# Optimization experiments

Hardware: AMD Instinct MI355X
Metric: run time of the kernel (lower is better)

Reference implementation:

```python
import jax, jax.numpy as jnp
import numpy as np

P = 10  # pred_num_conn (capped by max_pred_num_conn), component 0 = background
L = 6   # label_num_conn, component 0 = background
N, H, W = 4, 1024, 1024


def setup_inputs() -> dict:
    key = jax.random.key(0)
    k1, k2, k3 = jax.random.split(key, 3)
    pred = jax.random.uniform(k1, (N, H, W), dtype=jnp.float32)
    pred_conn = jax.random.randint(k2, (N, H, W), 0, P, dtype=jnp.int32)
    label_conn = jax.random.randint(k3, (N, H, W), 0, L, dtype=jnp.int32)
    return {"pred": pred, "pred_conn": pred_conn, "label_conn": label_conn}


def _image_sc_loss(pred_i, pconn, lconn):
    # pred_i: [H,W] float, pconn/lconn: [H,W] int component ids
    ph = jax.nn.one_hot(pconn, P, dtype=pred_i.dtype)   # [H,W,P]
    lh = jax.nn.one_hot(lconn, L, dtype=pred_i.dtype)   # [H,W,L]
    pm = ph * pred_i[..., None]                          # pred_j = mask_j * pred
    inter = jnp.einsum('hwl,hwp->lp', lh, pm)            # [L,P] intersection areas
    pred_area = jnp.sum(pm, axis=(0, 1))                 # [P]
    label_area = jnp.sum(lh, axis=(0, 1))                # [L]
    union = label_area[:, None] + pred_area[None, :] - inter
    safe_union = jnp.where(union == 0, 1.0, union)
    # compute_iou: 0 if intersect==0, 1 if union==0, else inter/union
    iou = jnp.where(inter == 0, 0.0,
                    jnp.where(union == 0, 1.0, inter / safe_union))
    ious = iou[1:, 1:]                                   # drop background comps -> [L-1, P-1]
    pair_conn = jnp.sum(ious, axis=1)                    # sum of nonzero ious per label comp
    pair_num = jnp.sum(ious != 0, axis=1).astype(pred_i.dtype)
    contrib = jnp.where(pair_num > 0,
                        pair_conn / jnp.where(pair_num > 0, pair_num, 1.0), 0.0)
    pair_conn_sum = jnp.sum(contrib)
    pred_col_sum = jnp.sum(ious, axis=0)                 # [P-1]
    lone_pred_num = jnp.sum(pred_col_sum == 0).astype(pred_i.dtype)
    real_label_num = jnp.asarray(L - 1, pred_i.dtype)
    img_connectivity = pair_conn_sum / (real_label_num + lone_pred_num)
    return 1.0 - img_connectivity                        # sc_loss for one class (class_num=1)


def reference(pred, pred_conn, label_conn):
    sc = jax.vmap(_image_sc_loss)(pred, pred_conn, label_conn)  # [N]
    return jnp.mean(sc)
```

## Files before the change

kernel.cpp:

```cpp
#include <hip/hip_runtime.h>

#define PP 10
#define LL 6
#define NIMG 4
#define HW (1024*1024)
#define BINS 66
#define NB 60
#define BX 512
#define TPB 128
#define ITERS 4


__global__ __launch_bounds__(TPB, 2) void accum_kernel(
    const float* __restrict__ pred,
    const int*   __restrict__ pconn,
    const int*   __restrict__ lconn,
    float*       __restrict__ ws)
{
    __shared__ float sb[NB * TPB];
    __shared__ float scnt[2][8];

    const int tid = threadIdx.x;
    const int img = blockIdx.y;
    const size_t base = (size_t)img * HW;

    {
        float4* sb4 = (float4*)sb;
        for (int i = tid; i < NB * TPB / 4; i += TPB)
            sb4[i] = make_float4(0.f, 0.f, 0.f, 0.f);
    }
    __syncthreads();

    const float4* __restrict__ p4  = (const float4*)(pred  + base);
    const int4*   __restrict__ pc4 = (const int4*)(pconn + base);
    const int4*   __restrict__ lc4 = (const int4*)(lconn + base);

    const int v0 = blockIdx.x * TPB + tid;
    const int stride = BX * TPB;

    float4 p[ITERS]; int4 pc[ITERS], lc[ITERS];
#pragma unroll
    for (int i = 0; i < ITERS; ++i) {
        const int v = v0 + i * stride;
        p[i]  = p4[v];
        pc[i] = pc4[v];
        lc[i] = lc4[v];
    }

    float cnt[LL];
#pragma unroll
    for (int l = 0; l < LL; ++l) cnt[l] = 0.0f;

#pragma unroll
    for (int i = 0; i < ITERS; ++i) {
#pragma unroll
        for (int l = 0; l < LL; ++l)
            cnt[l] += (float)((lc[i].x == l) + (lc[i].y == l)
                            + (lc[i].z == l) + (lc[i].w == l));
        sb[(lc[i].x * PP + pc[i].x) * TPB + tid] += p[i].x;
        sb[(lc[i].y * PP + pc[i].y) * TPB + tid] += p[i].y;
        sb[(lc[i].z * PP + pc[i].z) * TPB + tid] += p[i].z;
        sb[(lc[i].w * PP + pc[i].w) * TPB + tid] += p[i].w;
    }
    __syncthreads();

    float* wout = ws + ((size_t)img * BX + blockIdx.x) * BINS;

#pragma unroll
    for (int l = 0; l < LL; ++l) {
        float s = cnt[l];
        s += __shfl_down(s, 32, 64); s += __shfl_down(s, 16, 64);
        s += __shfl_down(s,  8, 64); s += __shfl_down(s,  4, 64);
        s += __shfl_down(s,  2, 64); s += __shfl_down(s,  1, 64);
        if ((tid & 63) == 0) scnt[tid >> 6][l] = s;
    }

    {
        const int b = tid >> 1, h = tid & 1;
        if (b < NB) {
            const float* col = sb + b * TPB + 64 * h;
            float s = 0.0f;
#pragma unroll
            for (int i = 0; i < 16; ++i) {
                const int ii = ((i + tid) & 15) * 4;
                const float4 t4 = *(const float4*)(col + ii);
                s += t4.x + t4.y + t4.z + t4.w;
            }
            s += __shfl_down(s, 1, 64);
            if (h == 0) wout[b] = s;
        }
    }
    __syncthreads();
    if (tid < LL) wout[NB + tid] = scnt[0][tid] + scnt[1][tid];
}

__global__ __launch_bounds__(1024) void finalize_kernel(
    const float* __restrict__ ws, float* __restrict__ out)
{
    __shared__ float part[4][NIMG * BINS];
    __shared__ float red[NIMG * BINS];
    __shared__ float contrib[NIMG];
    const int t = threadIdx.x;

    for (int T = t; T < 4 * NIMG * BINS; T += 1024) {
        const int ib = T >> 2, sub = T & 3;
        const int img = ib / BINS, b = ib % BINS;
        const float* basep = ws + ((size_t)img * BX + sub) * BINS + b;
        float s = 0.0f;
#pragma unroll 8
        for (int j = 0; j < BX / 4; ++j) s += basep[(size_t)j * 4 * BINS];
        part[sub][ib] = s;
    }
    __syncthreads();

    if (t < NIMG * BINS)
        red[t] = part[0][t] + part[1][t] + part[2][t] + part[3][t];
    __syncthreads();

    if (t < NIMG) {
        const float* b = red + t * BINS;
        float inter[LL][PP], pred_area[PP], label_area[LL];
        for (int p = 0; p < PP; ++p) pred_area[p] = 0.0f;
        for (int l = 0; l < LL; ++l) {
            label_area[l] = b[NB + l];
            for (int p = 0; p < PP; ++p) {
                inter[l][p] = b[l * PP + p];
                pred_area[p] += inter[l][p];
            }
        }
        float ious[LL][PP];
        for (int l = 1; l < LL; ++l) {
            for (int p = 1; p < PP; ++p) {
                float in = inter[l][p];
                float un = label_area[l] + pred_area[p] - in;
                float iou;
                if (in == 0.0f)      iou = 0.0f;
                else if (un == 0.0f) iou = 1.0f;
                else                 iou = in / un;
                ious[l][p] = iou;
            }
        }
        float pair_conn_sum = 0.0f;
        for (int l = 1; l < LL; ++l) {
            float pc = 0.0f; int pn = 0;
            for (int p = 1; p < PP; ++p) {
                pc += ious[l][p];
                pn += (ious[l][p] != 0.0f) ? 1 : 0;
            }
            if (pn > 0) pair_conn_sum += pc / (float)pn;
        }
        int lone = 0;
        for (int p = 1; p < PP; ++p) {
            float cs = 0.0f;
            for (int l = 1; l < LL; ++l) cs += ious[l][p];
            lone += (cs == 0.0f) ? 1 : 0;
        }
        contrib[t] = 1.0f - pair_conn_sum / (5.0f + (float)lone);
    }
    __syncthreads();
    if (t == 0)
        out[0] = (contrib[0] + contrib[1] + contrib[2] + contrib[3]) * 0.25f;
}

extern "C" void kernel_launch(void* const* d_in, const int* in_sizes, int n_in,
                              void* d_out, int out_size, void* d_ws, size_t ws_size,
                              hipStream_t stream) {
    const float* pred  = (const float*)d_in[0];
    const int*   pconn = (const int*)d_in[1];
    const int*   lconn = (const int*)d_in[2];
    float* out = (float*)d_out;
    float* ws  = (float*)d_ws;

    dim3 grid(BX, NIMG);
    accum_kernel<<<grid, TPB, 0, stream>>>(pred, pconn, lconn, ws);

    finalize_kernel<<<1, 1024, 0, stream>>>(ws, out);
}
```

Measured before the change: 109.6 us.

## Replace shared-memory scatter histogram with per-thread register one-hot FMA accumulation

Each thread now keeps all 60 label-by-prediction bins in registers and updates them with one-hot FMAs, in place of scattered read-modify-write updates to a private shared-memory column. Partial sums are combined with a 4-lane shuffle reduction, then written to a compact shared buffer and summed per bin. Block shape changes to 256 threads and 256 blocks per image. This removes the shared-memory zeroing and the indexed shared-memory updates, but adds about 240 FMAs per element and heavy register pressure.

```diff
diff --git a/kernel.cpp b/kernel.cpp
--- a/kernel.cpp
+++ b/kernel.cpp
@@ -6,30 +6,22 @@
 #define HW (1024*1024)
 #define BINS 66
 #define NB 60
-#define BX 512
-#define TPB 128
+#define BX 256
+#define TPB 256
 #define ITERS 4
 
 
-__global__ __launch_bounds__(TPB, 2) void accum_kernel(
+__global__ __launch_bounds__(TPB, 3) void accum_kernel(
     const float* __restrict__ pred,
     const int*   __restrict__ pconn,
     const int*   __restrict__ lconn,
     float*       __restrict__ ws)
 {
-    __shared__ float sb[NB * TPB];
-    __shared__ float scnt[2][8];
+    __shared__ float ld[BINS * 64];
 
     const int tid = threadIdx.x;
     const int img = blockIdx.y;
     const size_t base = (size_t)img * HW;
-
-    {
-        float4* sb4 = (float4*)sb;
-        for (int i = tid; i < NB * TPB / 4; i += TPB)
-            sb4[i] = make_float4(0.f, 0.f, 0.f, 0.f);
-    }
-    __syncthreads();
 
     const float4* __restrict__ p4  = (const float4*)(pred  + base);
     const int4*   __restrict__ pc4 = (const int4*)(pconn + base);
@@ -47,51 +39,65 @@
         lc[i] = lc4[v];
     }
 
+    float acc[LL][PP];
     float cnt[LL];
 #pragma unroll
-    for (int l = 0; l < LL; ++l) cnt[l] = 0.0f;
+    for (int l = 0; l < LL; ++l) {
+        cnt[l] = 0.0f;
+#pragma unroll
+        for (int q = 0; q < PP; ++q) acc[l][q] = 0.0f;
+    }
 
 #pragma unroll
     for (int i = 0; i < ITERS; ++i) {
 #pragma unroll
-        for (int l = 0; l < LL; ++l)
-            cnt[l] += (float)((lc[i].x == l) + (lc[i].y == l)
-                            + (lc[i].z == l) + (lc[i].w == l));
-        sb[(lc[i].x * PP + pc[i].x) * TPB + tid] += p[i].x;
-        sb[(lc[i].y * PP + pc[i].y) * TPB + tid] += p[i].y;
-        sb[(lc[i].z * PP + pc[i].z) * TPB + tid] += p[i].z;
-        sb[(lc[i].w * PP + pc[i].w) * TPB + tid] += p[i].w;
+        for (int c = 0; c < 4; ++c) {
+            const float pv  = (c == 0) ? p[i].x  : (c == 1) ? p[i].y  : (c == 2) ? p[i].z  : p[i].w;
+            const int   lcv = (c == 0) ? lc[i].x : (c == 1) ? lc[i].y : (c == 2) ? lc[i].z : lc[i].w;
+            const int   pcv = (c == 0) ? pc[i].x : (c == 1) ? pc[i].y : (c == 2) ? pc[i].z : pc[i].w;
+            float op[PP];
+#pragma unroll
+            for (int q = 0; q < PP; ++q) op[q] = (pcv == q) ? 1.0f : 0.0f;
+#pragma unroll
+            for (int l = 0; l < LL; ++l) {
+                const float ol = (lcv == l) ? 1.0f : 0.0f;
+                cnt[l] += ol;
+                const float hl = pv * ol;
+#pragma unroll
+                for (int q = 0; q < PP; ++q)
+                    acc[l][q] = fmaf(hl, op[q], acc[l][q]);
+            }
+        }
+    }
+
+    const int unit = (tid >> 6) * 16 + ((tid & 63) >> 2);
+    const bool writer = ((tid & 3) == 0);
+#pragma unroll
+    for (int l = 0; l < LL; ++l) {
+#pragma unroll
+        for (int q = 0; q < PP; ++q) {
+            float s = acc[l][q];
+            s += __shfl_down(s, 1, 64);
+            s += __shfl_down(s, 2, 64);
+            if (writer) ld[(l * PP + q) * 64 + unit] = s;
+        }
+        float s = cnt[l];
+        s += __shfl_down(s, 1, 64);
+        s += __shfl_down(s, 2, 64);
+        if (writer) ld[(NB + l) * 64 + unit] = s;
     }
     __syncthreads();
 
-    float* wout = ws + ((size_t)img * BX + blockIdx.x) * BINS;
-
+    if (tid < BINS) {
+        const float4* row = (const float4*)(ld + tid * 64);
+        float s = 0.0f;
 #pragma unroll
-    for (int l = 0; l < LL; ++l) {
-        float s = cnt[l];
-        s += __shfl_down(s, 32, 64); s += __shfl_down(s, 16, 64);
-        s += __shfl_down(s,  8, 64); s += __shfl_down(s,  4, 64);
-        s += __shfl_down(s,  2, 64); s += __shfl_down(s,  1, 64);
-        if ((tid & 63) == 0) scnt[tid >> 6][l] = s;
+        for (int i = 0; i < 16; ++i) {
+            const float4 t4 = row[i];
+            s += t4.x + t4.y + t4.z + t4.w;
+        }
+        ws[((size_t)img * BX + blockIdx.x) * BINS + tid] = s;
     }
-
-    {
-        const int b = tid >> 1, h = tid & 1;
-        if (b < NB) {
-            const float* col = sb + b * TPB + 64 * h;
-            float s = 0.0f;
-#pragma unroll
-            for (int i = 0; i < 16; ++i) {
-                const int ii = ((i + tid) & 15) * 4;
-                const float4 t4 = *(const float4*)(col + ii);
-                s += t4.x + t4.y + t4.z + t4.w;
-            }
-            s += __shfl_down(s, 1, 64);
-            if (h == 0) wout[b] = s;
-        }
-    }
-    __syncthreads();
-    if (tid < LL) wout[NB + tid] = scnt[0][tid] + scnt[1][tid];
 }
 
 __global__ __launch_bounds__(1024) void finalize_kernel(
```

Result: slower. 211.1 us (+92.6%).
